# Performance work log

Hardware: AMD Instinct MI355X
Metric: run time of the kernel (lower is better)

The kernel has to match this reference:

```python
import jax, jax.numpy as jnp
import numpy as np

AH, AW = 8, 8            # aligned_height, aligned_width
SCALE = 0.0625           # spatial_scale = 1/16
IMG = 1024               # image size implied by 64x64 feature map at stride 16


def setup_inputs() -> dict:
    key = jax.random.key(0)
    k1, k2, k3, k4, k5 = jax.random.split(key, 5)
    B, C, H, W = 4, 256, 64, 64
    N = 2000
    features = jax.random.normal(k1, (B, C, H, W), dtype=jnp.float32)
    # ROIs: (batch_idx, x1, y1, x2, y2) in image coordinates
    bidx = jax.random.randint(k2, (N,), 0, B).astype(jnp.float32)
    cx = jax.random.uniform(k3, (N,), minval=0.0, maxval=IMG)
    cy = jax.random.uniform(k4, (N,), minval=0.0, maxval=IMG)
    wh = jax.random.uniform(k5, (N, 2), minval=32.0, maxval=512.0)
    x1 = jnp.clip(cx - wh[:, 0] / 2, 0.0, IMG - 1.0)
    y1 = jnp.clip(cy - wh[:, 1] / 2, 0.0, IMG - 1.0)
    x2 = jnp.clip(cx + wh[:, 0] / 2, x1 + 16.0, float(IMG))
    y2 = jnp.clip(cy + wh[:, 1] / 2, y1 + 16.0, float(IMG))
    rois = jnp.stack([bidx, x1, y1, x2, y2], axis=1).astype(jnp.float32)
    return {"features": features, "rois": rois}


def _roi_align(features, rois):
    # Classic RoIAlign (crop_and_resize style): one bilinear sample per output
    # cell, sample grid spans the ROI with (aligned-1) intervals.
    B, C, H, W = features.shape
    N = rois.shape[0]
    b = rois[:, 0].astype(jnp.int32)
    x1 = rois[:, 1] * SCALE
    y1 = rois[:, 2] * SCALE
    x2 = rois[:, 3] * SCALE
    y2 = rois[:, 4] * SCALE
    bin_h = (y2 - y1) / (AH - 1.0)
    bin_w = (x2 - x1) / (AW - 1.0)
    ys = y1[:, None, None] + bin_h[:, None, None] * jnp.arange(AH, dtype=jnp.float32)[None, :, None]
    xs = x1[:, None, None] + bin_w[:, None, None] * jnp.arange(AW, dtype=jnp.float32)[None, None, :]
    ys = jnp.broadcast_to(ys, (N, AH, AW))
    xs = jnp.broadcast_to(xs, (N, AH, AW))
    valid = (ys >= 0) & (ys < H) & (xs >= 0) & (xs < W)
    y0 = jnp.floor(ys)
    x0 = jnp.floor(xs)
    ly = ys - y0  # bilinear weights
    lx = xs - x0
    iy0 = jnp.clip(y0.astype(jnp.int32), 0, H - 1)
    ix0 = jnp.clip(x0.astype(jnp.int32), 0, W - 1)
    iy1 = jnp.clip(iy0 + 1, 0, H - 1)
    ix1 = jnp.clip(ix0 + 1, 0, W - 1)
    bb = b[:, None, None]

    def g(iy, ix):
        return features[bb, :, iy, ix]  # [N, AH, AW, C]

    ly_ = ly[..., None]
    lx_ = lx[..., None]
    v = ((1 - ly_) * (1 - lx_) * g(iy0, ix0)
         + (1 - ly_) * lx_ * g(iy0, ix1)
         + ly_ * (1 - lx_) * g(iy1, ix0)
         + ly_ * lx_ * g(iy1, ix1))
    v = jnp.where(valid[..., None], v, 0.0)
    return jnp.transpose(v, (0, 3, 1, 2))  # [N, C, AH, AW]


def _max_pool_2x2_s1(x):
    # max_pool2d(kernel_size=2, stride=1): [N,C,h,w] -> [N,C,h-1,w-1]
    return jnp.maximum(
        jnp.maximum(x[:, :, :-1, :-1], x[:, :, :-1, 1:]),
        jnp.maximum(x[:, :, 1:, :-1], x[:, :, 1:, 1:]),
    )


def reference(features, rois):
    x = _roi_align(features, rois)
    return _max_pool_2x2_s1(x)  # [N, C, AH-1, AW-1]
```

## Files before the change

### kernel.cpp

```cpp
#include <hip/hip_runtime.h>
#include <cstdint>

constexpr int CCH = 256;
constexpr int HH  = 64;
constexpr int WW  = 64;
constexpr int OHW = 49;
constexpr float RSCALE = 0.0625f;

#define FMUL __fmul_rn
#define FADD __fadd_rn
#define FSUB __fsub_rn
#define FDIV __fdiv_rn

__device__ __forceinline__ float4 f4max(float4 a, float4 b) {
  return make_float4(fmaxf(a.x, b.x), fmaxf(a.y, b.y),
                     fmaxf(a.z, b.z), fmaxf(a.w, b.w));
}

__device__ __forceinline__ unsigned short f2bf(float f) {
  union { float f; unsigned u; } a; a.f = f;
  unsigned u = a.u;
  u += 0x7fffu + ((u >> 16) & 1u);
  return (unsigned short)(u >> 16);
}

__device__ __forceinline__ float4 bf4_to_f4(uint2 u) {
  float4 r;
  r.x = __uint_as_float(u.x << 16);
  r.y = __uint_as_float(u.x & 0xffff0000u);
  r.z = __uint_as_float(u.y << 16);
  r.w = __uint_as_float(u.y & 0xffff0000u);
  return r;
}

__global__ __launch_bounds__(256) void ktransbf(const float* __restrict__ in,
                                                unsigned short* __restrict__ out) {
  __shared__ float tile[64][65];
  const int b  = blockIdx.z;
  const int c0 = blockIdx.y * 64;
  const int s0 = blockIdx.x * 64;
  const int t  = threadIdx.x;
  const float* inb = in + (size_t)b * CCH * (HH * WW);
  unsigned short* outb = out + (size_t)b * (HH * WW) * CCH;

  const int cl = t >> 4, sq = t & 15;
#pragma unroll
  for (int k = 0; k < 4; ++k) {
    const int c = cl + 16 * k;
    const float4 v = *(const float4*)(inb + (size_t)(c0 + c) * (HH * WW) + s0 + 4 * sq);
    tile[c][4 * sq + 0] = v.x;
    tile[c][4 * sq + 1] = v.y;
    tile[c][4 * sq + 2] = v.z;
    tile[c][4 * sq + 3] = v.w;
  }
  __syncthreads();
  const int cq = t & 15, rl = t >> 4;
#pragma unroll
  for (int k = 0; k < 4; ++k) {
    const int r = rl + 16 * k;
    ushort4 w;
    w.x = f2bf(tile[4 * cq + 0][r]);
    w.y = f2bf(tile[4 * cq + 1][r]);
    w.z = f2bf(tile[4 * cq + 2][r]);
    w.w = f2bf(tile[4 * cq + 3][r]);
    *(ushort4*)(outb + (size_t)(s0 + r) * CCH + c0 + 4 * cq) = w;
  }
}

__global__ __launch_bounds__(256) void ksched(const float* __restrict__ rois,
                                              int N, int* __restrict__ meta) {
  __shared__ int cnt[4], rnk[4], off[4], slack[4], excess[4];
  const int t = threadIdx.x;
  if (t < 4) { cnt[t] = 0; rnk[t] = 0; }
  __syncthreads();
  for (int i = t; i < N; i += 256) atomicAdd(&cnt[(int)rois[i * 5]], 1);
  __syncthreads();
  if (t == 0) {
    const int full = N >> 3, rem = N & 7;
    int o = 0, cs = 0, ce = 0;
    for (int p = 0; p < 4; ++p) {
      off[p] = o; o += cnt[p];
      int rp = rem - 2 * p; rp = rp < 0 ? 0 : (rp > 2 ? 2 : rp);
      const int slots = 2 * full + rp;
      slack[p]  = cs; if (slots - cnt[p] > 0) cs += slots - cnt[p];
      excess[p] = ce; if (cnt[p] - slots > 0) ce += cnt[p] - slots;
      meta[p] = cnt[p]; meta[4 + p] = off[p]; meta[8 + p] = slack[p];
    }
  }
  __syncthreads();
  int* perm = meta + 16;
  for (int i = t; i < N; i += 256) {
    const int b = (int)rois[i * 5];
    perm[off[b] + atomicAdd(&rnk[b], 1)] = i;
  }
  __syncthreads();
  int* extra = meta + 16 + N;
  const int full = N >> 3, rem = N & 7;
  for (int p = 0; p < 4; ++p) {
    int rp = rem - 2 * p; rp = rp < 0 ? 0 : (rp > 2 ? 2 : rp);
    const int slots = 2 * full + rp;
    const int ex = cnt[p] - slots;
    for (int e = t; e < ex; e += 256) extra[excess[p] + e] = perm[off[p] + slots + e];
  }
}

__global__ __launch_bounds__(512, 3) void roi_kernel6(const uint2* __restrict__ feat,
                                                      const float* __restrict__ rois,
                                                      const int* __restrict__ meta,
                                                      int N, int use_perm,
                                                      float* __restrict__ out) {
  __shared__ float4 smem4[CCH * OHW / 4];
  float* smem = (float*)smem4;
  const int i  = blockIdx.x;
  const int t  = threadIdx.x;
  const int cg = t & 63;
  const int w  = t >> 6;

  int n = i;
  if (use_perm) {
    const int p   = (i & 7) >> 1;
    const int s   = (i >> 3) * 2 + (i & 1);
    const int c_  = meta[p];
    const int o_  = meta[4 + p];
    const int sl  = meta[8 + p];
    const int* perm  = meta + 16;
    const int* extra = meta + 16 + N;
    n = (s < c_) ? perm[o_ + s] : extra[sl + (s - c_)];
  }

  const float rb = rois[n * 5 + 0];
  const float x1 = FMUL(rois[n * 5 + 1], RSCALE);
  const float y1 = FMUL(rois[n * 5 + 2], RSCALE);
  const float x2 = FMUL(rois[n * 5 + 3], RSCALE);
  const float y2 = FMUL(rois[n * 5 + 4], RSCALE);
  const int   b  = (int)rb;
  const float bh = FDIV(FSUB(y2, y1), 7.0f);
  const float bw = FDIV(FSUB(x2, x1), 7.0f);

  int   xo0[8], xo1[8];
  float lx[8];
  bool  xv[8];
#pragma unroll
  for (int q = 0; q < 8; ++q) {
    const float xs = FADD(x1, FMUL(bw, (float)q));
    xv[q] = (xs >= 0.0f) && (xs < (float)WW);
    const float xf = floorf(xs);
    lx[q] = FSUB(xs, xf);
    int a = (int)xf;
    a = a < 0 ? 0 : (a > WW - 1 ? WW - 1 : a);
    xo0[q] = a * (CCH / 4);
    xo1[q] = ((a + 1 > WW - 1) ? WW - 1 : a + 1) * (CCH / 4);
  }

  const float ys = FADD(y1, FMUL(bh, (float)w));
  const bool  yv = (ys >= 0.0f) && (ys < (float)HH);
  const float yf = floorf(ys);
  const float ly = FSUB(ys, yf);
  int d = (int)yf;
  d = d < 0 ? 0 : (d > HH - 1 ? HH - 1 : d);
  const int d1 = (d + 1 > HH - 1) ? HH - 1 : d + 1;

  const uint2* fb = feat + (size_t)b * (HH * WW) * (CCH / 4) + cg;
  const uint2* r0 = fb + (size_t)d  * (WW * (CCH / 4));
  const uint2* r1 = fb + (size_t)d1 * (WW * (CCH / 4));
  const float wy1 = ly, wy0 = 1.0f - ly;

  float4 hc[7], vprev;
#pragma unroll
  for (int h = 0; h < 2; ++h) {
    uint2 g00[4], g01[4], g10[4], g11[4];
#pragma unroll
    for (int q = 0; q < 4; ++q) {
      const int s = 4 * h + q;
      g00[q] = r0[xo0[s]];
      g01[q] = r0[xo1[s]];
      g10[q] = r1[xo0[s]];
      g11[q] = r1[xo1[s]];
    }
    float4 v[4];
#pragma unroll
    for (int q = 0; q < 4; ++q) {
      const int s = 4 * h + q;
      const bool ok = yv && xv[s];
      const float wx1 = lx[s], wx0 = 1.0f - wx1;
      const float a00 = wy0 * wx0, a01 = wy0 * wx1;
      const float a10 = wy1 * wx0, a11 = wy1 * wx1;
      const float4 f00 = bf4_to_f4(g00[q]);
      const float4 f01 = bf4_to_f4(g01[q]);
      const float4 f10 = bf4_to_f4(g10[q]);
      const float4 f11 = bf4_to_f4(g11[q]);
      float4 r;
      r.x = a00 * f00.x + a01 * f01.x + a10 * f10.x + a11 * f11.x;
      r.y = a00 * f00.y + a01 * f01.y + a10 * f10.y + a11 * f11.y;
      r.z = a00 * f00.z + a01 * f01.z + a10 * f10.z + a11 * f11.z;
      r.w = a00 * f00.w + a01 * f01.w + a10 * f10.w + a11 * f11.w;
      v[q] = ok ? r : make_float4(0.f, 0.f, 0.f, 0.f);
    }
    if (h == 0) {
      hc[0] = f4max(v[0], v[1]);
      hc[1] = f4max(v[1], v[2]);
      hc[2] = f4max(v[2], v[3]);
      vprev = v[3];
    } else {
      hc[3] = f4max(vprev, v[0]);
      hc[4] = f4max(v[0], v[1]);
      hc[5] = f4max(v[1], v[2]);
      hc[6] = f4max(v[2], v[3]);
    }
  }

  if (w >= 1) {
#pragma unroll
    for (int m = 0; m < 7; ++m)
      smem4[((w - 1) * 7 + m) * 64 + cg] = hc[m];
  }
  __syncthreads();

  if (w <= 6) {
#pragma unroll
    for (int m = 0; m < 7; ++m)
      hc[m] = f4max(hc[m], smem4[(w * 7 + m) * 64 + cg]);
  }
  __syncthreads();

  if (w <= 6) {
#pragma unroll
    for (int m = 0; m < 7; ++m) {
      const int s  = w * 7 + m;
      const int gp = cg ^ ((s >> 2) & 7);
      smem4[s * (CCH / 4) + gp] = hc[m];
    }
  }
  __syncthreads();

  float4* o4 = (float4*)(out + (size_t)n * (CCH * OHW));
#pragma unroll
  for (int m = 0; m < 7; ++m) {
    const int idx = m * 512 + t;
    if (idx < (CCH * OHW) / 4) {
      const int f0 = idx * 4;
      float4 wv;
      float* wp = (float*)&wv;
#pragma unroll
      for (int k = 0; k < 4; ++k) {
        const int e = f0 + k;
        const int c = e / 49;
        const int s = e - c * 49;
        wp[k] = smem[s * CCH + 4 * ((c >> 2) ^ ((s >> 2) & 7)) + (c & 3)];
      }
      o4[idx] = wv;
    }
  }
}

__global__ __launch_bounds__(256) void roi_kernel_fb(const float* __restrict__ feat,
                                                     const float* __restrict__ rois,
                                                     float* __restrict__ out) {
  __shared__ float sout[CCH * OHW];
  const int n = blockIdx.x;
  const int c = threadIdx.x;

  const float rb = rois[n * 5 + 0];
  const float x1 = FMUL(rois[n * 5 + 1], RSCALE);
  const float y1 = FMUL(rois[n * 5 + 2], RSCALE);
  const float x2 = FMUL(rois[n * 5 + 3], RSCALE);
  const float y2 = FMUL(rois[n * 5 + 4], RSCALE);
  const int b = (int)rb;
  const float bh = FDIV(FSUB(y2, y1), 7.0f);
  const float bw = FDIV(FSUB(x2, x1), 7.0f);

  int ix0[8], ix1[8], iy0[8], iy1[8];
  float lx[8], ly[8];
  bool xv[8], yv[8];
#pragma unroll
  for (int i = 0; i < 8; ++i) {
    const float xs = FADD(x1, FMUL(bw, (float)i));
    const float ys = FADD(y1, FMUL(bh, (float)i));
    xv[i] = (xs >= 0.0f) && (xs < (float)WW);
    yv[i] = (ys >= 0.0f) && (ys < (float)HH);
    const float xf = floorf(xs);
    const float yf = floorf(ys);
    lx[i] = FSUB(xs, xf);
    ly[i] = FSUB(ys, yf);
    int a = (int)xf;
    a = a < 0 ? 0 : (a > WW - 1 ? WW - 1 : a);
    ix0[i] = a;
    ix1[i] = (a + 1 > WW - 1) ? WW - 1 : a + 1;
    int d = (int)yf;
    d = d < 0 ? 0 : (d > HH - 1 ? HH - 1 : d);
    iy0[i] = d;
    iy1[i] = (d + 1 > HH - 1) ? HH - 1 : d + 1;
  }

  const float* fbp = feat + ((size_t)b * CCH + c) * (size_t)(HH * WW);
  float hp[7];
#pragma unroll
  for (int j = 0; j < 8; ++j) {
    float v[8];
    const float wy1 = ly[j], wy0 = 1.0f - ly[j];
#pragma unroll
    for (int i = 0; i < 8; ++i) {
      if (yv[j] && xv[i]) {
        const float f00 = fbp[iy0[j] * WW + ix0[i]];
        const float f01 = fbp[iy0[j] * WW + ix1[i]];
        const float f10 = fbp[iy1[j] * WW + ix0[i]];
        const float f11 = fbp[iy1[j] * WW + ix1[i]];
        const float wx1 = lx[i], wx0 = 1.0f - wx1;
        v[i] = wy0 * (wx0 * f00 + wx1 * f01) + wy1 * (wx0 * f10 + wx1 * f11);
      } else {
        v[i] = 0.0f;
      }
    }
    float hc[7];
#pragma unroll
    for (int i = 0; i < 7; ++i) hc[i] = fmaxf(v[i], v[i + 1]);
    if (j > 0) {
#pragma unroll
      for (int i = 0; i < 7; ++i)
        sout[c * OHW + (j - 1) * 7 + i] = fmaxf(hp[i], hc[i]);
    }
#pragma unroll
    for (int i = 0; i < 7; ++i) hp[i] = hc[i];
  }
  __syncthreads();
  const float4* s4 = (const float4*)sout;
  float4* o4 = (float4*)(out + (size_t)n * (CCH * OHW));
  for (int q = c; q < (CCH * OHW) / 4; q += 256) o4[q] = s4[q];
}

extern "C" void kernel_launch(void* const* d_in, const int* in_sizes, int n_in,
                              void* d_out, int out_size, void* d_ws, size_t ws_size,
                              hipStream_t stream) {
  (void)n_in; (void)out_size;
  const float* feat = (const float*)d_in[0];
  const float* rois = (const float*)d_in[1];
  float* out = (float*)d_out;
  const int N = in_sizes[1] / 5;
  const int B = in_sizes[0] / (CCH * HH * WW);
  const size_t featbf_bytes = (size_t)in_sizes[0] * sizeof(unsigned short);
  const size_t meta_bytes   = (size_t)(16 + 2 * N) * sizeof(int);

  if (ws_size >= featbf_bytes + meta_bytes) {
    unsigned short* featbf = (unsigned short*)d_ws;
    int* meta = (int*)((char*)d_ws + featbf_bytes);
    const int use_perm = (B == 4) ? 1 : 0;

    ktransbf<<<dim3((HH * WW) / 64, CCH / 64, B), dim3(256), 0, stream>>>(
        feat, featbf);
    if (use_perm)
      ksched<<<dim3(1), dim3(256), 0, stream>>>(rois, N, meta);
    roi_kernel6<<<dim3(N), dim3(512), 0, stream>>>(
        (const uint2*)featbf, rois, meta, N, use_perm, out);
  } else {
    roi_kernel_fb<<<dim3(N), dim3(256), 0, stream>>>(feat, rois, out);
  }
}
```

Before: 140.2 us.

## Split each ROI across two 256-thread blocks by channel half with nontemporal stores

Each ROI is now handled by two 256-thread blocks, each covering half of the 256 channels, in place of one 512-thread block. This halves the shared memory per block and raises the launch-bounds occupancy target. The batch-interleaved scheduling is adjusted so each of the 4 batch partitions gets M/8 slots, with a fallback when M is not a multiple of 8. Output writes switch to nontemporal vector stores to reduce cache pollution. The cost is that ROI coordinate math is duplicated across the two blocks, and each half-block now writes smaller contiguous output chunks.

```diff
diff --git a/kernel.cpp b/kernel.cpp
--- a/kernel.cpp
+++ b/kernel.cpp
@@ -11,6 +11,8 @@
 #define FADD __fadd_rn
 #define FSUB __fsub_rn
 #define FDIV __fdiv_rn
+
+typedef float v4f __attribute__((ext_vector_type(4)));
 
 __device__ __forceinline__ float4 f4max(float4 a, float4 b) {
   return make_float4(fmaxf(a.x, b.x), fmaxf(a.y, b.y),
@@ -68,7 +70,8 @@
 }
 
 __global__ __launch_bounds__(256) void ksched(const float* __restrict__ rois,
-                                              int N, int* __restrict__ meta) {
+                                              int N, int slots,
+                                              int* __restrict__ meta) {
   __shared__ int cnt[4], rnk[4], off[4], slack[4], excess[4];
   const int t = threadIdx.x;
   if (t < 4) { cnt[t] = 0; rnk[t] = 0; }
@@ -76,12 +79,9 @@
   for (int i = t; i < N; i += 256) atomicAdd(&cnt[(int)rois[i * 5]], 1);
   __syncthreads();
   if (t == 0) {
-    const int full = N >> 3, rem = N & 7;
     int o = 0, cs = 0, ce = 0;
     for (int p = 0; p < 4; ++p) {
       off[p] = o; o += cnt[p];
-      int rp = rem - 2 * p; rp = rp < 0 ? 0 : (rp > 2 ? 2 : rp);
-      const int slots = 2 * full + rp;
       slack[p]  = cs; if (slots - cnt[p] > 0) cs += slots - cnt[p];
       excess[p] = ce; if (cnt[p] - slots > 0) ce += cnt[p] - slots;
       meta[p] = cnt[p]; meta[4 + p] = off[p]; meta[8 + p] = slack[p];
@@ -95,37 +95,37 @@
   }
   __syncthreads();
   int* extra = meta + 16 + N;
-  const int full = N >> 3, rem = N & 7;
   for (int p = 0; p < 4; ++p) {
-    int rp = rem - 2 * p; rp = rp < 0 ? 0 : (rp > 2 ? 2 : rp);
-    const int slots = 2 * full + rp;
     const int ex = cnt[p] - slots;
     for (int e = t; e < ex; e += 256) extra[excess[p] + e] = perm[off[p] + slots + e];
   }
 }
 
-__global__ __launch_bounds__(512, 3) void roi_kernel6(const uint2* __restrict__ feat,
+__global__ __launch_bounds__(256, 6) void roi_kernel7(const uint2* __restrict__ feat,
                                                       const float* __restrict__ rois,
                                                       const int* __restrict__ meta,
                                                       int N, int use_perm,
                                                       float* __restrict__ out) {
-  __shared__ float4 smem4[CCH * OHW / 4];
+  __shared__ float4 smem4[OHW * 32];
   float* smem = (float*)smem4;
-  const int i  = blockIdx.x;
-  const int t  = threadIdx.x;
-  const int cg = t & 63;
-  const int w  = t >> 6;
-
-  int n = i;
+  const int i = blockIdx.x;
+  const int t = threadIdx.x;
+  const int g = t & 31;
+  const int r = t >> 5;
+
+  int n, half;
   if (use_perm) {
-    const int p   = (i & 7) >> 1;
-    const int s   = (i >> 3) * 2 + (i & 1);
-    const int c_  = meta[p];
-    const int o_  = meta[4 + p];
-    const int sl  = meta[8 + p];
+    const int p = (i & 7) >> 1;
+    half        = i & 1;
+    const int s = i >> 3;
+    const int c_ = meta[p];
+    const int o_ = meta[4 + p];
+    const int sl = meta[8 + p];
     const int* perm  = meta + 16;
     const int* extra = meta + 16 + N;
     n = (s < c_) ? perm[o_ + s] : extra[sl + (s - c_)];
+  } else {
+    n = i >> 1; half = i & 1;
   }
 
   const float rb = rois[n * 5 + 0];
@@ -152,7 +152,7 @@
     xo1[q] = ((a + 1 > WW - 1) ? WW - 1 : a + 1) * (CCH / 4);
   }
 
-  const float ys = FADD(y1, FMUL(bh, (float)w));
+  const float ys = FADD(y1, FMUL(bh, (float)r));
   const bool  yv = (ys >= 0.0f) && (ys < (float)HH);
   const float yf = floorf(ys);
   const float ly = FSUB(ys, yf);
@@ -160,7 +160,7 @@
   d = d < 0 ? 0 : (d > HH - 1 ? HH - 1 : d);
   const int d1 = (d + 1 > HH - 1) ? HH - 1 : d + 1;
 
-  const uint2* fb = feat + (size_t)b * (HH * WW) * (CCH / 4) + cg;
+  const uint2* fb = feat + (size_t)b * (HH * WW) * (CCH / 4) + (half * 32 + g);
   const uint2* r0 = fb + (size_t)d  * (WW * (CCH / 4));
   const uint2* r1 = fb + (size_t)d1 * (WW * (CCH / 4));
   const float wy1 = ly, wy0 = 1.0f - ly;
@@ -189,12 +189,12 @@
       const float4 f01 = bf4_to_f4(g01[q]);
       const float4 f10 = bf4_to_f4(g10[q]);
       const float4 f11 = bf4_to_f4(g11[q]);
-      float4 r;
-      r.x = a00 * f00.x + a01 * f01.x + a10 * f10.x + a11 * f11.x;
-      r.y = a00 * f00.y + a01 * f01.y + a10 * f10.y + a11 * f11.y;
-      r.z = a00 * f00.z + a01 * f01.z + a10 * f10.z + a11 * f11.z;
-      r.w = a00 * f00.w + a01 * f01.w + a10 * f10.w + a11 * f11.w;
-      v[q] = ok ? r : make_float4(0.f, 0.f, 0.f, 0.f);
+      float4 rr;
+      rr.x = a00 * f00.x + a01 * f01.x + a10 * f10.x + a11 * f11.x;
+      rr.y = a00 * f00.y + a01 * f01.y + a10 * f10.y + a11 * f11.y;
+      rr.z = a00 * f00.z + a01 * f01.z + a10 * f10.z + a11 * f11.z;
+      rr.w = a00 * f00.w + a01 * f01.w + a10 * f10.w + a11 * f11.w;
+      v[q] = ok ? rr : make_float4(0.f, 0.f, 0.f, 0.f);
     }
     if (h == 0) {
       hc[0] = f4max(v[0], v[1]);
@@ -209,46 +209,45 @@
     }
   }
 
-  if (w >= 1) {
+  if (r >= 1) {
 #pragma unroll
     for (int m = 0; m < 7; ++m)
-      smem4[((w - 1) * 7 + m) * 64 + cg] = hc[m];
-  }
-  __syncthreads();
-
-  if (w <= 6) {
+      smem4[((r - 1) * 7 + m) * 32 + g] = hc[m];
+  }
+  __syncthreads();
+
+  if (r <= 6) {
 #pragma unroll
     for (int m = 0; m < 7; ++m)
-      hc[m] = f4max(hc[m], smem4[(w * 7 + m) * 64 + cg]);
-  }
-  __syncthreads();
-
-  if (w <= 6) {
+      hc[m] = f4max(hc[m], smem4[(r * 7 + m) * 32 + g]);
+  }
+  __syncthreads();
+
+  if (r <= 6) {
 #pragma unroll
     for (int m = 0; m < 7; ++m) {
-      const int s  = w * 7 + m;
-      const int gp = cg ^ ((s >> 2) & 7);
-      smem4[s * (CCH / 4) + gp] = hc[m];
-    }
-  }
-  __syncthreads();
-
-  float4* o4 = (float4*)(out + (size_t)n * (CCH * OHW));
+      const int s  = r * 7 + m;
+      const int gp = g ^ ((s >> 2) & 7);
+      smem4[s * 32 + gp] = hc[m];
+    }
+  }
+  __syncthreads();
+
+  v4f* o4 = (v4f*)(out + (size_t)n * (CCH * OHW) + half * (CCH / 2) * OHW);
 #pragma unroll
   for (int m = 0; m < 7; ++m) {
-    const int idx = m * 512 + t;
-    if (idx < (CCH * OHW) / 4) {
+    const int idx = m * 256 + t;
+    if (idx < (CCH / 2) * OHW / 4) {
       const int f0 = idx * 4;
-      float4 wv;
-      float* wp = (float*)&wv;
+      v4f wv;
 #pragma unroll
       for (int k = 0; k < 4; ++k) {
         const int e = f0 + k;
         const int c = e / 49;
         const int s = e - c * 49;
-        wp[k] = smem[s * CCH + 4 * ((c >> 2) ^ ((s >> 2) & 7)) + (c & 3)];
+        wv[k] = smem[s * 128 + 4 * ((c >> 2) ^ ((s >> 2) & 7)) + (c & 3)];
       }
-      o4[idx] = wv;
+      __builtin_nontemporal_store(wv, &o4[idx]);
     }
   }
 }
@@ -337,19 +336,20 @@
   float* out = (float*)d_out;
   const int N = in_sizes[1] / 5;
   const int B = in_sizes[0] / (CCH * HH * WW);
+  const int M = 2 * N;
   const size_t featbf_bytes = (size_t)in_sizes[0] * sizeof(unsigned short);
   const size_t meta_bytes   = (size_t)(16 + 2 * N) * sizeof(int);
 
   if (ws_size >= featbf_bytes + meta_bytes) {
     unsigned short* featbf = (unsigned short*)d_ws;
     int* meta = (int*)((char*)d_ws + featbf_bytes);
-    const int use_perm = (B == 4) ? 1 : 0;
+    const int use_perm = (B == 4 && (M & 7) == 0) ? 1 : 0;
 
     ktransbf<<<dim3((HH * WW) / 64, CCH / 64, B), dim3(256), 0, stream>>>(
         feat, featbf);
     if (use_perm)
-      ksched<<<dim3(1), dim3(256), 0, stream>>>(rois, N, meta);
-    roi_kernel6<<<dim3(N), dim3(512), 0, stream>>>(
+      ksched<<<dim3(1), dim3(256), 0, stream>>>(rois, N, M >> 3, meta);
+    roi_kernel7<<<dim3(M), dim3(256), 0, stream>>>(
         (const uint2*)featbf, rois, meta, N, use_perm, out);
   } else {
     roi_kernel_fb<<<dim3(N), dim3(256), 0, stream>>>(feat, rois, out);
```

Result: faster. 137.4 us (-2.0%).
